# Kernel optimization log

Hardware: AMD Instinct MI355X
Metric: run time of the kernel (lower is better)

## Reference

```python
import jax, jax.numpy as jnp
import numpy as np

B, T, N, D, H, MH = 8, 13, 128, 4, 64, 128


def setup_inputs() -> dict:
    key = jax.random.key(0)
    ks = iter(jax.random.split(key, 32))
    def w(shape):
        return (jax.random.normal(next(ks), shape, jnp.float32) / np.sqrt(shape[0])).astype(jnp.float32)
    def b(n):
        return jnp.zeros((n,), jnp.float32)
    return {
        "A": jax.random.normal(next(ks), (B, N, N), jnp.float32),
        "X": jax.random.normal(next(ks), (B, T, N, D), jnp.float32),
        "Wm1": w((2 * H, MH)), "bm1": b(MH),
        "Wm2": w((MH, H)), "bm2": b(H),
        "Wir": w((D, H)), "bir": b(H),
        "Wii": w((D, H)), "bii": b(H),
        "Win": w((D, H)), "bin_": b(H),
        "Whr": w((H, H)), "Whi": w((H, H)), "Whh": w((H, H)),
        "Wmr": w((H, H)), "Wmi": w((H, H)), "Wmn": w((H, H)),
        "Wo1": w((H, H)), "bo1": b(H),
        "Wo2": w((H, H)), "bo2": b(H),
        "Wo3": w((H, D)), "bo3": b(D),
        "log_sigma": jnp.log(jnp.float32(0.1)),
    }


def _project_adjacency(A, temp=1.0, eps=1e-6):
    A = 0.5 * (A + jnp.swapaxes(A, -1, -2))
    A = jax.nn.sigmoid(A / temp)
    n = A.shape[-1]
    A = A * (1.0 - jnp.eye(n, dtype=A.dtype))
    return A / (A.sum(axis=-1, keepdims=True) + eps)


def reference(A, X, Wm1, bm1, Wm2, bm2, Wir, bir, Wii, bii, Win, bin_,
              Whr, Whi, Whh, Wmr, Wmi, Wmn, Wo1, bo1, Wo2, bo2, Wo3, bo3, log_sigma):
    Ap = _project_adjacency(A)
    Bb, Tt, Nn, Dd = X.shape
    Hh = Whr.shape[0]
    sigma = jnp.clip(jnp.exp(log_sigma), 1e-4, 10.0)
    count = Bb * Nn * Dd
    const = 0.5 * count * jnp.log(2.0 * jnp.pi * sigma * sigma)
    inv2s2 = 1.0 / (2.0 * sigma * sigma)

    def step(carry, xt_tgt):
        hidden, ll = carry
        x_t, tgt = xt_tgt
        # all-pairs message: pre[b,i,j] = [h_i, h_j]
        pre = jnp.concatenate([
            jnp.broadcast_to(hidden[:, :, None, :], (Bb, Nn, Nn, Hh)),
            jnp.broadcast_to(hidden[:, None, :, :], (Bb, Nn, Nn, Hh)),
        ], axis=-1)
        msg = jnp.tanh(jnp.tanh(pre @ Wm1 + bm1) @ Wm2 + bm2)
        # agg[b,j] = sum_i A[b,i,j] * msg[b,i,j]
        agg = jnp.einsum('bij,bijh->bjh', Ap, msg)
        r = jax.nn.sigmoid(x_t @ Wir + bir + hidden @ Whr + agg @ Wmr)
        i = jax.nn.sigmoid(x_t @ Wii + bii + hidden @ Whi + agg @ Wmi)
        n = jnp.tanh(x_t @ Win + bin_ + r * (hidden @ Whh) + agg @ Wmn)
        h_new = (1.0 - i) * n + i * hidden
        pred = jax.nn.relu(h_new @ Wo1 + bo1)
        pred = jax.nn.relu(pred @ Wo2 + bo2)
        pred = x_t + pred @ Wo3 + bo3
        nll = const + jnp.sum((tgt - pred) ** 2) * inv2s2
        return (h_new, ll - nll), pred

    hidden0 = jnp.zeros((Bb, Nn, Hh), X.dtype)
    xs = (jnp.moveaxis(X[:, :-1], 1, 0), jnp.moveaxis(X[:, 1:], 1, 0))  # time-major
    (_, loglik), preds = jax.lax.scan(step, (hidden0, jnp.float32(0.0)), xs)
    X_pred = jnp.moveaxis(preds, 0, 1)  # [B, T-1, N, D]
    return (X_pred, loglik)
```

## Files before the change

### kernel.cpp

```cpp
#include <hip/hip_runtime.h>
#include <math.h>

#define B_ 8
#define N_ 128
#define H_ 64
#define MH_ 128
#define D_ 4
#define TSTEPS 12
#define NBLK 256

typedef __attribute__((ext_vector_type(8))) short bf16x8;
typedef __attribute__((ext_vector_type(4))) float f32x4;
typedef __attribute__((ext_vector_type(4))) unsigned u32x4;
typedef unsigned uint32;

__device__ __forceinline__ float fast_tanh(float x) {
    float t = __builtin_amdgcn_exp2f(x * 2.8853900817779268f);
    return 1.0f - 2.0f * __builtin_amdgcn_rcpf(t + 1.0f);
}
__device__ __forceinline__ float fast_sigmoid(float x) {
    float t = __builtin_amdgcn_exp2f(x * -1.4426950408889634f);
    return __builtin_amdgcn_rcpf(1.0f + t);
}
__device__ __forceinline__ unsigned short f2bf(float x) {
    unsigned u = __builtin_bit_cast(unsigned, x);
    u += 0x7fffu + ((u >> 16) & 1u);
    return (unsigned short)(u >> 16);
}
__device__ __forceinline__ uint32 cvtpk(float lo, float hi) {
    uint32 r;
    asm("v_cvt_pk_bf16_f32 %0, %1, %2" : "=v"(r) : "v"(lo), "v"(hi));
    return r;
}

constexpr int PB_STRIDE = 65536;
constexpr int CTRLu = 11 * PB_STRIDE;
constexpr int CTRL_BYTES = (32 * 16 + 2) * 4;

__global__ __launch_bounds__(1024, 4) void fused(
    const float* __restrict__ A, const float* __restrict__ X,
    const float* __restrict__ Wm1, const float* __restrict__ bm1,
    const float* __restrict__ Wm2, const float* __restrict__ bm2,
    const float* __restrict__ Wir, const float* __restrict__ bir,
    const float* __restrict__ Wii, const float* __restrict__ bii,
    const float* __restrict__ Win, const float* __restrict__ bin_,
    const float* __restrict__ Whr, const float* __restrict__ Whi, const float* __restrict__ Whh,
    const float* __restrict__ Wmr, const float* __restrict__ Wmi, const float* __restrict__ Wmn,
    const float* __restrict__ Wo1, const float* __restrict__ bo1,
    const float* __restrict__ Wo2, const float* __restrict__ bo2,
    const float* __restrict__ Wo3, const float* __restrict__ bo3,
    const float* __restrict__ lsg,
    uint32* wsU, float* __restrict__ out)
{
    __shared__ __align__(16) unsigned short wm2f[8192];
    __shared__ __align__(16) float WamL[12288];
    __shared__ __align__(16) float Wm1L[16384];
    __shared__ float Qj[4][128], apRow[4][128], rs[128], bmS[128];
    __shared__ float aggbuf[4][4][64];
    __shared__ float sAgg[4][64], sAm[4][192];
    __shared__ float sH[4][64], sHn[4][64], sHP[4][192];
    __shared__ float sT1[4][64], sT2[4][64];
    __shared__ float sX[4][4], sTgt[4][4], sSq[4][4], sseb[1];

    const int bid = blockIdx.x, tid = threadIdx.x;
    const int b = bid >> 5;
    const int j0 = (bid & 31) << 2;
    const int wave = tid >> 6, lane = tid & 63;
    const int jj = wave >> 2;
    const int wvj = wave & 3;
    const int l15 = lane & 15, g = lane >> 4;
    const int myI0 = wvj * 32;

    int*   cntBase = (int*)(wsU + CTRLu);
    int*   cntW    = cntBase + (b * 4 + wvj) * 16;
    int*   cntPub  = cntBase + (b * 4 + (j0 >> 5)) * 16;
    float* sseG    = (float*)(wsU + CTRLu + 512);
    int*   doneG   = (int*)(wsU + CTRLu + 513);
    const float* Ab = A + b * 16384;

    {
        int i = tid & 127, q = tid >> 7;
        float part = 0.f;
        int jlo = q * 16;
        #pragma unroll 4
        for (int j2 = jlo; j2 < jlo + 16; ++j2)
            if (j2 != i)
                part += fast_sigmoid(0.5f * (Ab[i * 128 + j2] + Ab[j2 * 128 + i]));
        ((float*)aggbuf)[q * 128 + i] = part;
    }
    __syncthreads();
    if (tid < 128) {
        const float* f = (const float*)aggbuf;
        float s = 0.f;
        #pragma unroll
        for (int c = 0; c < 8; ++c) s += f[c * 128 + tid];
        rs[tid] = s + 1e-6f;
        bmS[tid] = bm1[tid];
    }
    __syncthreads();
    if (tid < 512) {
        int i = tid & 127, h = tid >> 7, jc = j0 + h;
        float s = (i == jc) ? 0.f
                : fast_sigmoid(0.5f * (Ab[i * 128 + jc] + Ab[jc * 128 + i]));
        apRow[h][i] = s / rs[i];
    }
    for (int idx = tid; idx < 8192; idx += 1024) {
        int kt = idx >> 11, nt = (idx >> 9) & 3, ln = (idx >> 3) & 63, e = idx & 7;
        int k = kt * 32 + (ln >> 4) * 8 + e, n = nt * 16 + (ln & 15);
        wm2f[idx] = f2bf(Wm2[k * 64 + n]);
    }
    for (int idx = tid; idx < 12288; idx += 1024) {
        int k = idx / 192, c = idx % 192;
        WamL[idx] = ((c < 64) ? Wmr : (c < 128) ? Wmi : Wmn)[k * 64 + (c & 63)];
    }
    for (int idx = tid; idx < 16384; idx += 1024)
        Wm1L[idx] = Wm1[idx];
    if (tid < 512) Qj[tid >> 7][tid & 127] = 0.f;
    if (tid < 256) sH[tid >> 6][tid & 63] = 0.f;
    if (tid < 768) sHP[tid / 192][tid % 192] = 0.f;
    if (tid == 0) sseb[0] = 0.f;
    __syncthreads();

    for (int t = 0; t < TSTEPS; ++t) {
        const uint32* Psrc = wsU + (t - 1) * PB_STRIDE + b * 8192;
        if (t > 0) {
            const int target = 32 * t;
            int guard = 0;
            while (__hip_atomic_load(cntW, __ATOMIC_RELAXED, __HIP_MEMORY_SCOPE_AGENT) < target
                   && guard < (1 << 20)) {
                __builtin_amdgcn_s_sleep(1);
                ++guard;
            }
            __builtin_amdgcn_fence(__ATOMIC_ACQUIRE, "workgroup");
        }

        f32x4 acc[2][4];
        #pragma unroll
        for (int mt = 0; mt < 2; ++mt)
            #pragma unroll
            for (int nt = 0; nt < 4; ++nt) {
                f32x4 z = {0.f, 0.f, 0.f, 0.f};
                acc[mt][nt] = z;
            }
        #pragma unroll
        for (int kt = 0; kt < 4; ++kt) {
            int k0 = kt * 32 + g * 8;
            bf16x8 bf[4];
            #pragma unroll
            for (int nt = 0; nt < 4; ++nt)
                bf[nt] = *(const bf16x8*)&wm2f[((kt * 4 + nt) * 64 + lane) << 3];
            f32x4 qa = *(const f32x4*)&Qj[jj][k0];
            f32x4 qb = *(const f32x4*)&Qj[jj][k0 + 4];
            bf16x8 af[2];
            #pragma unroll
            for (int mt = 0; mt < 2; ++mt) {
                int row = myI0 + mt * 16 + l15;
                float pe[8];
                if (t > 0) {
                    u32x4 pv = *(const u32x4*)(Psrc + row * 64 + kt * 16 + g * 4);
                    #pragma unroll
                    for (int c = 0; c < 4; ++c) {
                        pe[2 * c]     = __builtin_bit_cast(float, pv[c] << 16);
                        pe[2 * c + 1] = __builtin_bit_cast(float, pv[c] & 0xFFFF0000u);
                    }
                } else {
                    #pragma unroll
                    for (int e = 0; e < 8; ++e) pe[e] = bmS[k0 + e];
                }
                float tv[8];
                #pragma unroll
                for (int e = 0; e < 4; ++e) {
                    tv[e]     = fast_tanh(pe[e] + qa[e]);
                    tv[4 + e] = fast_tanh(pe[4 + e] + qb[e]);
                }
                u32x4 aw;
                aw[0] = cvtpk(tv[0], tv[1]); aw[1] = cvtpk(tv[2], tv[3]);
                aw[2] = cvtpk(tv[4], tv[5]); aw[3] = cvtpk(tv[6], tv[7]);
                af[mt] = __builtin_bit_cast(bf16x8, aw);
            }
            #pragma unroll
            for (int mt = 0; mt < 2; ++mt)
                #pragma unroll
                for (int nt = 0; nt < 4; ++nt)
                    acc[mt][nt] = __builtin_amdgcn_mfma_f32_16x16x32_bf16(af[mt], bf[nt], acc[mt][nt], 0, 0, 0);
        }
        {
            float bmv[4];
            #pragma unroll
            for (int nt = 0; nt < 4; ++nt) bmv[nt] = bm2[nt * 16 + l15];
            float pagg[4] = {0.f, 0.f, 0.f, 0.f};
            #pragma unroll
            for (int mt = 0; mt < 2; ++mt) {
                float w[4];
                #pragma unroll
                for (int v = 0; v < 4; ++v) w[v] = apRow[jj][myI0 + mt * 16 + g * 4 + v];
                #pragma unroll
                for (int nt = 0; nt < 4; ++nt)
                    #pragma unroll
                    for (int v = 0; v < 4; ++v)
                        pagg[nt] += w[v] * fast_tanh(acc[mt][nt][v] + bmv[nt]);
            }
            #pragma unroll
            for (int nt = 0; nt < 4; ++nt) {
                pagg[nt] += __shfl_xor(pagg[nt], 16);
                pagg[nt] += __shfl_xor(pagg[nt], 32);
            }
            if (lane < 16)
                #pragma unroll
                for (int nt = 0; nt < 4; ++nt) aggbuf[jj][wvj][nt * 16 + lane] = pagg[nt];
        }
        __syncthreads();
        if (tid < 256) {
            int r = tid >> 6, o = tid & 63;
            sAgg[r][o] = aggbuf[r][0][o] + aggbuf[r][1][o] + aggbuf[r][2][o] + aggbuf[r][3][o];
        }
        if (tid < 16) {
            int r = tid >> 2, d = tid & 3, jrow = j0 + r;
            sX[r][d]   = X[((b * 13 + t) * 128 + jrow) * 4 + d];
            sTgt[r][d] = X[((b * 13 + t + 1) * 128 + jrow) * 4 + d];
        }
        __syncthreads();

        if (tid < 384) {
            int pr = tid / 192, c = tid % 192;
            int r0 = pr * 2, r1 = r0 + 1;
            float a0 = 0.f, a1 = 0.f;
            #pragma unroll 8
            for (int k = 0; k < 64; ++k) {
                float w = WamL[k * 192 + c];
                a0 += sAgg[r0][k] * w; a1 += sAgg[r1][k] * w;
            }
            sAm[r0][c] = a0; sAm[r1][c] = a1;
        }
        __syncthreads();
        if (tid < 256) {
            int r = tid >> 6, o = tid & 63;
            float xr = bir[o], xi = bii[o], xn = bin_[o];
            #pragma unroll
            for (int d = 0; d < 4; ++d) {
                float xv = sX[r][d];
                xr += xv * Wir[d * 64 + o];
                xi += xv * Wii[d * 64 + o];
                xn += xv * Win[d * 64 + o];
            }
            float rr = fast_sigmoid(xr + sHP[r][o]       + sAm[r][o]);
            float ig = fast_sigmoid(xi + sHP[r][64 + o]  + sAm[r][64 + o]);
            float nn = fast_tanh  (xn + rr * sHP[r][128 + o] + sAm[r][128 + o]);
            float hn = (1.0f - ig) * nn + ig * sH[r][o];
            sHn[r][o] = hn; sH[r][o] = hn;
        }
        __syncthreads();

        const bool lastT = (t == TSTEPS - 1);
        if (tid < 128 || (tid >= 512 && tid < 640)) {
            if (!lastT) {
                int hi2 = (tid >= 512) ? 1 : 0;
                int o = tid - hi2 * 512;
                int r0 = hi2 * 2, r1 = r0 + 1;
                float a0 = bmS[o], a1 = bmS[o];
                #pragma unroll 8
                for (int k = 0; k < 64; ++k) {
                    float w = Wm1L[k * 128 + o];
                    a0 += sHn[r0][k] * w; a1 += sHn[r1][k] * w;
                }
                uint32 u0 = cvtpk(a0, __shfl_down(a0, 1));
                uint32 u1 = cvtpk(a1, __shfl_down(a1, 1));
                if ((o & 1) == 0) {
                    uint32* base = wsU + t * PB_STRIDE + b * 8192;
                    __hip_atomic_store(base + (j0 + r0) * 64 + (o >> 1), u0,
                                       __ATOMIC_RELAXED, __HIP_MEMORY_SCOPE_AGENT);
                    __hip_atomic_store(base + (j0 + r1) * 64 + (o >> 1), u1,
                                       __ATOMIC_RELAXED, __HIP_MEMORY_SCOPE_AGENT);
                }
                asm volatile("s_waitcnt vmcnt(0)" ::: "memory");
                if (lane == 0)
                    __hip_atomic_fetch_add(cntPub, 1, __ATOMIC_RELAXED, __HIP_MEMORY_SCOPE_AGENT);
            }
        } else if (tid < 256 || (tid >= 640 && tid < 768)) {
            if (!lastT) {
                int hi2 = (tid >= 640) ? 1 : 0;
                int oo = tid - 128 - hi2 * 512;
                int r0 = hi2 * 2, r1 = r0 + 1;
                float a0 = 0.f, a1 = 0.f;
                #pragma unroll 8
                for (int k = 0; k < 64; ++k) {
                    float w = Wm1L[(64 + k) * 128 + oo];
                    a0 += sHn[r0][k] * w; a1 += sHn[r1][k] * w;
                }
                Qj[r0][oo] = a0; Qj[r1][oo] = a1;
            }
        } else if (tid < 448 || (tid >= 768 && tid < 960)) {
            if (!lastT) {
                int hi2 = (tid >= 768) ? 1 : 0;
                int c = tid - 256 - hi2 * 512;
                int r0 = hi2 * 2, r1 = r0 + 1;
                const float* W = (c < 64) ? Whr : (c < 128) ? Whi : Whh;
                int oc = c & 63;
                float a0 = 0.f, a1 = 0.f;
                #pragma unroll 8
                for (int k = 0; k < 64; ++k) {
                    float w = W[k * 64 + oc];
                    a0 += sHn[r0][k] * w; a1 += sHn[r1][k] * w;
                }
                sHP[r0][c] = a0; sHP[r1][c] = a1;
            }
        } else {
            int hi2 = (tid >= 960) ? 1 : 0;
            int o = tid - 448 - hi2 * 512;
            int r0 = hi2 * 2, r1 = r0 + 1;
            float a0 = bo1[o], a1 = a0;
            #pragma unroll 8
            for (int k = 0; k < 64; ++k) {
                float w = Wo1[k * 64 + o];
                a0 += sHn[r0][k] * w; a1 += sHn[r1][k] * w;
            }
            sT1[r0][o] = fmaxf(a0, 0.f); sT1[r1][o] = fmaxf(a1, 0.f);
        }
        __syncthreads();
        if (tid < 256) {
            int r = tid >> 6, o = tid & 63;
            float a = bo2[o];
            #pragma unroll 8
            for (int k = 0; k < 64; ++k) a += sT1[r][k] * Wo2[k * 64 + o];
            sT2[r][o] = fmaxf(a, 0.f);
        }
        __syncthreads();
        if (tid < 64) {
            int r = tid >> 4, d = (tid >> 2) & 3, q = tid & 3;
            float a = 0.f;
            #pragma unroll 4
            for (int k = q * 16; k < q * 16 + 16; ++k) a += sT2[r][k] * Wo3[k * 4 + d];
            a += __shfl_xor(a, 1);
            a += __shfl_xor(a, 2);
            if (q == 0) {
                float p = sX[r][d] + a + bo3[d];
                out[((b * TSTEPS + t) * 128 + (j0 + r)) * 4 + d] = p;
                float df = sTgt[r][d] - p;
                sSq[r][d] = df * df;
            }
        }
        __syncthreads();
        if (tid == 0) {
            float s = 0.f;
            #pragma unroll
            for (int r = 0; r < 4; ++r)
                #pragma unroll
                for (int d = 0; d < 4; ++d) s += sSq[r][d];
            sseb[0] += s;
        }
        __syncthreads();
    }

    if (tid == 0) atomicAdd(sseG, sseb[0]);
    __syncthreads();
    if (tid == 0) {
        int prev = __hip_atomic_fetch_add(doneG, 1, __ATOMIC_RELAXED, __HIP_MEMORY_SCOPE_AGENT);
        if (prev == NBLK - 1) {
            float sse = __hip_atomic_load(sseG, __ATOMIC_RELAXED, __HIP_MEMORY_SCOPE_AGENT);
            float ls = lsg[0];
            float sigma = fminf(fmaxf(expf(ls), 1e-4f), 10.0f);
            float c = 0.5f * 4096.0f * logf(2.0f * 3.14159265358979323846f * sigma * sigma);
            float inv2s2 = 1.0f / (2.0f * sigma * sigma);
            out[B_ * TSTEPS * N_ * D_] = -(12.0f * c + sse * inv2s2);
        }
    }
}

extern "C" void kernel_launch(void* const* d_in, const int* in_sizes, int n_in,
                              void* d_out, int out_size, void* d_ws, size_t ws_size,
                              hipStream_t stream)
{
    const float* A    = (const float*)d_in[0];
    const float* X    = (const float*)d_in[1];
    const float* Wm1  = (const float*)d_in[2];
    const float* bm1  = (const float*)d_in[3];
    const float* Wm2  = (const float*)d_in[4];
    const float* bm2  = (const float*)d_in[5];
    const float* Wir  = (const float*)d_in[6];
    const float* bir  = (const float*)d_in[7];
    const float* Wii  = (const float*)d_in[8];
    const float* bii  = (const float*)d_in[9];
    const float* Win  = (const float*)d_in[10];
    const float* bin_ = (const float*)d_in[11];
    const float* Whr  = (const float*)d_in[12];
    const float* Whi  = (const float*)d_in[13];
    const float* Whh  = (const float*)d_in[14];
    const float* Wmr  = (const float*)d_in[15];
    const float* Wmi  = (const float*)d_in[16];
    const float* Wmn  = (const float*)d_in[17];
    const float* Wo1  = (const float*)d_in[18];
    const float* bo1  = (const float*)d_in[19];
    const float* Wo2  = (const float*)d_in[20];
    const float* bo2  = (const float*)d_in[21];
    const float* Wo3  = (const float*)d_in[22];
    const float* bo3  = (const float*)d_in[23];
    const float* lsg  = (const float*)d_in[24];
    uint32* wsU = (uint32*)d_ws;
    float* out = (float*)d_out;

    hipMemsetAsync((char*)d_ws + (size_t)CTRLu * 4, 0, CTRL_BYTES, stream);

    hipLaunchKernelGGL(fused, dim3(NBLK), dim3(1024), 0, stream,
                       A, X, Wm1, bm1, Wm2, bm2, Wir, bir, Wii, bii, Win, bin_,
                       Whr, Whi, Whh, Wmr, Wmi, Wmn, Wo1, bo1, Wo2, bo2, Wo3, bo3,
                       lsg, wsU, out);
}
```

Measured before the change: 219.9 us.

## Defer output MLP out of the recurrent loop using stored hidden history

Stores every timestep's hidden state in a shared-memory history buffer and removes the three-layer output MLP, prediction write and SSE reduction from the serial per-timestep loop. After the loop, each wave computes the predictions for three (timestep,row) pairs in a batch, using per-wave scratch and wave-level reductions. This shortens the critical path of each recurrent step, which involves cross-block spin waits, and drops two block barriers per step. In exchange it adds 12 KB of shared memory and a serial post-loop phase.

```diff
diff --git a/kernel.cpp b/kernel.cpp
--- a/kernel.cpp
+++ b/kernel.cpp
@@ -57,10 +57,9 @@
     __shared__ __align__(16) float Wm1L[16384];
     __shared__ float Qj[4][128], apRow[4][128], rs[128], bmS[128];
     __shared__ float aggbuf[4][4][64];
-    __shared__ float sAgg[4][64], sAm[4][192];
-    __shared__ float sH[4][64], sHn[4][64], sHP[4][192];
-    __shared__ float sT1[4][64], sT2[4][64];
-    __shared__ float sX[4][4], sTgt[4][4], sSq[4][4], sseb[1];
+    __shared__ float sAgg[4][64], sAm[4][192], sHP[4][192];
+    __shared__ float sHist[TSTEPS][4][64];
+    __shared__ float sX[4][4];
 
     const int bid = blockIdx.x, tid = threadIdx.x;
     const int b = bid >> 5;
@@ -116,9 +115,7 @@
     for (int idx = tid; idx < 16384; idx += 1024)
         Wm1L[idx] = Wm1[idx];
     if (tid < 512) Qj[tid >> 7][tid & 127] = 0.f;
-    if (tid < 256) sH[tid >> 6][tid & 63] = 0.f;
     if (tid < 768) sHP[tid / 192][tid % 192] = 0.f;
-    if (tid == 0) sseb[0] = 0.f;
     __syncthreads();
 
     for (int t = 0; t < TSTEPS; ++t) {
@@ -216,8 +213,7 @@
         }
         if (tid < 16) {
             int r = tid >> 2, d = tid & 3, jrow = j0 + r;
-            sX[r][d]   = X[((b * 13 + t) * 128 + jrow) * 4 + d];
-            sTgt[r][d] = X[((b * 13 + t + 1) * 128 + jrow) * 4 + d];
+            sX[r][d] = X[((b * 13 + t) * 128 + jrow) * 4 + d];
         }
         __syncthreads();
 
@@ -243,17 +239,16 @@
                 xi += xv * Wii[d * 64 + o];
                 xn += xv * Win[d * 64 + o];
             }
+            float hprev = (t > 0) ? sHist[t - 1][r][o] : 0.f;
             float rr = fast_sigmoid(xr + sHP[r][o]       + sAm[r][o]);
             float ig = fast_sigmoid(xi + sHP[r][64 + o]  + sAm[r][64 + o]);
             float nn = fast_tanh  (xn + rr * sHP[r][128 + o] + sAm[r][128 + o]);
-            float hn = (1.0f - ig) * nn + ig * sH[r][o];
-            sHn[r][o] = hn; sH[r][o] = hn;
+            sHist[t][r][o] = (1.0f - ig) * nn + ig * hprev;
         }
         __syncthreads();
 
-        const bool lastT = (t == TSTEPS - 1);
-        if (tid < 128 || (tid >= 512 && tid < 640)) {
-            if (!lastT) {
+        if (t < TSTEPS - 1) {
+            if (tid < 128 || (tid >= 512 && tid < 640)) {
                 int hi2 = (tid >= 512) ? 1 : 0;
                 int o = tid - hi2 * 512;
                 int r0 = hi2 * 2, r1 = r0 + 1;
@@ -261,7 +256,7 @@
                 #pragma unroll 8
                 for (int k = 0; k < 64; ++k) {
                     float w = Wm1L[k * 128 + o];
-                    a0 += sHn[r0][k] * w; a1 += sHn[r1][k] * w;
+                    a0 += sHist[t][r0][k] * w; a1 += sHist[t][r1][k] * w;
                 }
                 uint32 u0 = cvtpk(a0, __shfl_down(a0, 1));
                 uint32 u1 = cvtpk(a1, __shfl_down(a1, 1));
@@ -275,9 +270,7 @@
                 asm volatile("s_waitcnt vmcnt(0)" ::: "memory");
                 if (lane == 0)
                     __hip_atomic_fetch_add(cntPub, 1, __ATOMIC_RELAXED, __HIP_MEMORY_SCOPE_AGENT);
-            }
-        } else if (tid < 256 || (tid >= 640 && tid < 768)) {
-            if (!lastT) {
+            } else if (tid < 256 || (tid >= 640 && tid < 768)) {
                 int hi2 = (tid >= 640) ? 1 : 0;
                 int oo = tid - 128 - hi2 * 512;
                 int r0 = hi2 * 2, r1 = r0 + 1;
@@ -285,12 +278,10 @@
                 #pragma unroll 8
                 for (int k = 0; k < 64; ++k) {
                     float w = Wm1L[(64 + k) * 128 + oo];
-                    a0 += sHn[r0][k] * w; a1 += sHn[r1][k] * w;
+                    a0 += sHist[t][r0][k] * w; a1 += sHist[t][r1][k] * w;
                 }
                 Qj[r0][oo] = a0; Qj[r1][oo] = a1;
-            }
-        } else if (tid < 448 || (tid >= 768 && tid < 960)) {
-            if (!lastT) {
+            } else if (tid < 448 || (tid >= 768 && tid < 960)) {
                 int hi2 = (tid >= 768) ? 1 : 0;
                 int c = tid - 256 - hi2 * 512;
                 int r0 = hi2 * 2, r1 = r0 + 1;
@@ -300,61 +291,65 @@
                 #pragma unroll 8
                 for (int k = 0; k < 64; ++k) {
                     float w = W[k * 64 + oc];
-                    a0 += sHn[r0][k] * w; a1 += sHn[r1][k] * w;
+                    a0 += sHist[t][r0][k] * w; a1 += sHist[t][r1][k] * w;
                 }
                 sHP[r0][c] = a0; sHP[r1][c] = a1;
             }
-        } else {
-            int hi2 = (tid >= 960) ? 1 : 0;
-            int o = tid - 448 - hi2 * 512;
-            int r0 = hi2 * 2, r1 = r0 + 1;
-            float a0 = bo1[o], a1 = a0;
+        }
+        __syncthreads();
+    }
+
+    float ssePart = 0.f;
+    {
+        float* scratch = &((float*)aggbuf)[wave * 64];
+        #pragma unroll
+        for (int inst = 0; inst < 3; ++inst) {
+            int idx = wave + (inst << 4);
+            int tt = idx >> 2, r = idx & 3;
+            float a = bo1[lane];
             #pragma unroll 8
-            for (int k = 0; k < 64; ++k) {
-                float w = Wo1[k * 64 + o];
-                a0 += sHn[r0][k] * w; a1 += sHn[r1][k] * w;
-            }
-            sT1[r0][o] = fmaxf(a0, 0.f); sT1[r1][o] = fmaxf(a1, 0.f);
-        }
-        __syncthreads();
-        if (tid < 256) {
-            int r = tid >> 6, o = tid & 63;
-            float a = bo2[o];
+            for (int k = 0; k < 64; ++k) a += sHist[tt][r][k] * Wo1[k * 64 + lane];
+            scratch[lane] = fmaxf(a, 0.f);
+            asm volatile("s_waitcnt lgkmcnt(0)" ::: "memory");
+            __builtin_amdgcn_sched_barrier(0);
+            float a2 = bo2[lane];
             #pragma unroll 8
-            for (int k = 0; k < 64; ++k) a += sT1[r][k] * Wo2[k * 64 + o];
-            sT2[r][o] = fmaxf(a, 0.f);
-        }
-        __syncthreads();
-        if (tid < 64) {
-            int r = tid >> 4, d = (tid >> 2) & 3, q = tid & 3;
-            float a = 0.f;
-            #pragma unroll 4
-            for (int k = q * 16; k < q * 16 + 16; ++k) a += sT2[r][k] * Wo3[k * 4 + d];
-            a += __shfl_xor(a, 1);
-            a += __shfl_xor(a, 2);
-            if (q == 0) {
-                float p = sX[r][d] + a + bo3[d];
-                out[((b * TSTEPS + t) * 128 + (j0 + r)) * 4 + d] = p;
-                float df = sTgt[r][d] - p;
-                sSq[r][d] = df * df;
-            }
-        }
-        __syncthreads();
-        if (tid == 0) {
-            float s = 0.f;
-            #pragma unroll
-            for (int r = 0; r < 4; ++r)
-                #pragma unroll
-                for (int d = 0; d < 4; ++d) s += sSq[r][d];
-            sseb[0] += s;
-        }
-        __syncthreads();
-    }
-
-    if (tid == 0) atomicAdd(sseG, sseb[0]);
+            for (int k = 0; k < 64; ++k) a2 += scratch[k] * Wo2[k * 64 + lane];
+            scratch[lane] = fmaxf(a2, 0.f);
+            asm volatile("s_waitcnt lgkmcnt(0)" ::: "memory");
+            __builtin_amdgcn_sched_barrier(0);
+            if (lane < 16) {
+                int d = lane >> 2, q = lane & 3;
+                float a3 = 0.f;
+                #pragma unroll 4
+                for (int k = q * 16; k < q * 16 + 16; ++k) a3 += scratch[k] * Wo3[k * 4 + d];
+                a3 += __shfl_xor(a3, 1);
+                a3 += __shfl_xor(a3, 2);
+                if (q == 0) {
+                    int jrow = j0 + r;
+                    float xv = X[((b * 13 + tt) * 128 + jrow) * 4 + d];
+                    float tg = X[((b * 13 + tt + 1) * 128 + jrow) * 4 + d];
+                    float p = xv + a3 + bo3[d];
+                    out[((b * TSTEPS + tt) * 128 + jrow) * 4 + d] = p;
+                    float df = tg - p;
+                    ssePart += df * df;
+                }
+            }
+            asm volatile("s_waitcnt lgkmcnt(0)" ::: "memory");
+            __builtin_amdgcn_sched_barrier(0);
+        }
+    }
+    #pragma unroll
+    for (int d = 1; d < 64; d <<= 1) ssePart += __shfl_xor(ssePart, d);
+    if (lane == 0) rs[wave] = ssePart;
     __syncthreads();
+
     if (tid == 0) {
-        int prev = __hip_atomic_fetch_add(doneG, 1, __ATOMIC_RELAXED, __HIP_MEMORY_SCOPE_AGENT);
+        float s = 0.f;
+        #pragma unroll
+        for (int w = 0; w < 16; ++w) s += rs[w];
+        atomicAdd(sseG, s);
+        int prev = __hip_atomic_fetch_add(doneG, 1, __ATOMIC_ACQ_REL, __HIP_MEMORY_SCOPE_AGENT);
         if (prev == NBLK - 1) {
             float sse = __hip_atomic_load(sseG, __ATOMIC_RELAXED, __HIP_MEMORY_SCOPE_AGENT);
             float ls = lsg[0];
```

New measurement: 199.0 us. -9.5%, faster.
